# Optimization experiments

Measured on AMD Instinct MI355X. Metric: run time of the kernel, lower is better.

## Reference

```python
import jax, jax.numpy as jnp
import numpy as np

N, E, D, G, L = 50000, 400000, 64, 256, 4
VA, VB = 64, 8   # atom / bond feature vocab sizes
NUM_ATOM_FEATS, NUM_BOND_FEATS = 9, 3
MSG_EPS = 1e-7   # GENConv message epsilon
LN_EPS = 1e-5


def layernorm(x, g, b):
    mu = x.mean(-1, keepdims=True)
    var = x.var(-1, keepdims=True)
    return (x - mu) * jax.lax.rsqrt(var + LN_EPS) * g + b


def genconv(h, edge_emb, src, dst, W, b):
    # GENConv (aggr='softmax', t=1, mlp_layers=1):
    # msg = relu(x_j + e) + eps; per-dst per-feature softmax-weighted sum; mlp(x + m)
    msg = jax.nn.relu(h[src] + edge_emb) + MSG_EPS          # [E, D]
    mmax = jax.ops.segment_max(msg, dst, num_segments=N)    # [N, D]
    mmax = jnp.where(jnp.isfinite(mmax), mmax, 0.0)         # nodes with no in-edges
    ex = jnp.exp(msg - mmax[dst])
    denom = jax.ops.segment_sum(ex, dst, num_segments=N)
    alpha = ex / jnp.maximum(denom[dst], 1e-16)
    m = jax.ops.segment_sum(alpha * msg, dst, num_segments=N)  # [N, D]
    return (h + m) @ W + b


def setup_inputs():
    key = jax.random.key(0)
    ks = jax.random.split(key, 10)
    x = jax.random.randint(ks[0], (N, NUM_ATOM_FEATS), 0, VA)
    edge_index = jax.random.randint(ks[1], (2, E), 0, N)
    edge_attr = jax.random.randint(ks[2], (E, NUM_BOND_FEATS), 0, VB)
    batch = jnp.sort(jax.random.randint(ks[3], (N,), 0, G))
    s = 0.02
    w = 1.0 / np.sqrt(D).astype(np.float32)
    atom_emb = jax.random.normal(ks[4], (NUM_ATOM_FEATS, VA, D), jnp.float32) * s
    bond_emb = jax.random.normal(ks[5], (NUM_BOND_FEATS, VB, D), jnp.float32) * s
    gcn_W = jax.random.normal(ks[6], (L, D, D), jnp.float32) * w
    gcn_b = jnp.zeros((L, D), jnp.float32)
    norm_g = jnp.ones((L, D), jnp.float32)
    norm_b = jnp.zeros((L, D), jnp.float32)
    vn_emb = jnp.zeros((1, D), jnp.float32)  # constant-init virtualnode embedding
    vn_W1 = jax.random.normal(ks[7], (L - 1, D, D), jnp.float32) * w
    vn_b1 = jnp.zeros((L - 1, D), jnp.float32)
    vn_g1 = jnp.ones((L - 1, D), jnp.float32)
    vn_be1 = jnp.zeros((L - 1, D), jnp.float32)
    vn_W2 = jax.random.normal(ks[8], (L - 1, D, D), jnp.float32) * w
    vn_b2 = jnp.zeros((L - 1, D), jnp.float32)
    vn_g2 = jnp.ones((L - 1, D), jnp.float32)
    vn_be2 = jnp.zeros((L - 1, D), jnp.float32)
    return dict(x=x, edge_index=edge_index, edge_attr=edge_attr, batch=batch,
                atom_emb=atom_emb, bond_emb=bond_emb, gcn_W=gcn_W, gcn_b=gcn_b,
                norm_g=norm_g, norm_b=norm_b, vn_emb=vn_emb,
                vn_W1=vn_W1, vn_b1=vn_b1, vn_g1=vn_g1, vn_be1=vn_be1,
                vn_W2=vn_W2, vn_b2=vn_b2, vn_g2=vn_g2, vn_be2=vn_be2)


def reference(x, edge_index, edge_attr, batch, atom_emb, bond_emb, gcn_W, gcn_b,
              norm_g, norm_b, vn_emb, vn_W1, vn_b1, vn_g1, vn_be1,
              vn_W2, vn_b2, vn_g2, vn_be2):
    src, dst = edge_index[0], edge_index[1]
    # AtomEncoder / BondEncoder: sum of per-feature embedding lookups
    h = atom_emb[jnp.arange(NUM_ATOM_FEATS)[None, :], x].sum(1)          # [N, D]
    edge_emb = bond_emb[jnp.arange(NUM_BOND_FEATS)[None, :], edge_attr].sum(1)  # [E, D]
    vn = jnp.broadcast_to(vn_emb[0], (G, D))
    h = h + vn[batch]
    # block == 'res+' (eval mode: dropout is identity)
    h = genconv(h, edge_emb, src, dst, gcn_W[0], gcn_b[0])
    for l in range(1, L):
        h2 = jax.nn.relu(layernorm(h, norm_g[l - 1], norm_b[l - 1]))
        vt = jax.ops.segment_sum(h2, batch, num_segments=G) + vn         # global_add_pool
        vt = jax.nn.relu(layernorm(vt @ vn_W1[l - 1] + vn_b1[l - 1], vn_g1[l - 1], vn_be1[l - 1]))
        vn = jax.nn.relu(layernorm(vt @ vn_W2[l - 1] + vn_b2[l - 1], vn_g2[l - 1], vn_be2[l - 1]))
        h2 = h2 + vn[batch]
        h = genconv(h2, edge_emb, src, dst, gcn_W[l], gcn_b[l]) + h
    return layernorm(h, norm_g[L - 1], norm_b[L - 1])
```

## Files before the change

kernel.cpp:

```cpp
#include <hip/hip_runtime.h>
#include <hip/hip_bf16.h>

typedef __hip_bfloat16 bf16;

#define GNUM 256
#define LN_EPS 1e-5f
#define MSG_EPS 1e-7f

typedef float f4v __attribute__((ext_vector_type(4)));
typedef short s8v __attribute__((ext_vector_type(8)));
typedef __bf16 b8v __attribute__((ext_vector_type(8)));

template <typename V>
__device__ auto mfma_bf16_(V a, V b, f4v c, int)
    -> decltype(__builtin_amdgcn_mfma_f32_16x16x32_bf16(a, b, c, 0, 0, 0)) {
  return __builtin_amdgcn_mfma_f32_16x16x32_bf16(a, b, c, 0, 0, 0);
}
template <typename V>
__device__ f4v mfma_bf16_(V a, V b, f4v c, long) {
  return __builtin_amdgcn_mfma_f32_16x16x32_bf16(__builtin_bit_cast(s8v, a),
                                                 __builtin_bit_cast(s8v, b), c, 0, 0, 0);
}
__device__ __forceinline__ f4v mfma16(uint4 a, uint4 b, f4v c){
  return mfma_bf16_(__builtin_bit_cast(b8v, a), __builtin_bit_cast(b8v, b), c, 0);
}

__device__ __forceinline__ float bu2f(unsigned short u){
  unsigned v = ((unsigned)u) << 16; return __builtin_bit_cast(float, v);
}
__device__ __forceinline__ unsigned short f2bu(float f){
  unsigned u = __builtin_bit_cast(unsigned, f);
  return (unsigned short)((u + 0x7FFFu + ((u >> 16) & 1u)) >> 16);
}

__device__ __forceinline__ float wave_sum64(float v){
  #pragma unroll
  for (int off = 32; off > 0; off >>= 1) v += __shfl_xor(v, off, 64);
  return v;
}

struct Params15 {
  const void* src[15];
  int n[15];
  int off[15];
};

__global__ __launch_bounds__(256) void k_convert(Params15 P, int* __restrict__ flag,
                                                 float* __restrict__ dst,
                                                 int* __restrict__ counts, int nc){
  __shared__ int isf_sh;
  int tid = threadIdx.x;
  if (tid < 64){
    const unsigned short* u = (const unsigned short*)P.src[0];
    int bad = 0;
    for (int k = tid; k < 256; k += 64){
      unsigned short v = u[2*k];
      if (((v >> 7) & 0xFFu) >= 137u) bad = 1;
    }
    unsigned long long m = __ballot(bad);
    if (tid == 0) isf_sh = (m != 0ull) ? 1 : 0;
  }
  __syncthreads();
  bool isf = (isf_sh != 0);
  if (blockIdx.x == 0 && tid == 0) *flag = isf ? 1 : 0;
  for (int a = 0; a < 15; ++a){
    int n = P.n[a];
    float* d = dst + P.off[a];
    if (isf){
      const float* s = (const float*)P.src[a];
      for (int i = blockIdx.x*256 + tid; i < n; i += gridDim.x*256) d[i] = s[i];
    } else {
      const bf16* s = (const bf16*)P.src[a];
      for (int i = blockIdx.x*256 + tid; i < n; i += gridDim.x*256) d[i] = __bfloat162float(s[i]);
    }
  }
  for (int i = blockIdx.x*256 + tid; i < nc; i += gridDim.x*256) counts[i] = 0;
}

__global__ void k_count(const int* __restrict__ dst, int* __restrict__ counts, int E){
  int e = blockIdx.x*256 + threadIdx.x;
  if (e < E) atomicAdd(counts + dst[e], 1);
}

__global__ __launch_bounds__(256) void k_scan1(const int* __restrict__ counts,
                                               int* __restrict__ offs,
                                               int* __restrict__ btot, int n){
  __shared__ int wsum[4];
  int tid = threadIdx.x, w = tid >> 6, lane = tid & 63;
  int i = blockIdx.x*256 + tid;
  int v = (i < n) ? counts[i] : 0;
  int incl = v;
  #pragma unroll
  for (int off = 1; off < 64; off <<= 1){
    int t = __shfl_up(incl, off, 64);
    if (lane >= off) incl += t;
  }
  if (lane == 63) wsum[w] = incl;
  __syncthreads();
  int woff = 0;
  for (int k = 0; k < w; ++k) woff += wsum[k];
  int tot = incl + woff;
  if (i < n) offs[i+1] = tot;
  if (tid == 255) btot[blockIdx.x] = tot;
}

__global__ __launch_bounds__(256) void k_scan2(const int* __restrict__ btot,
                                               int* __restrict__ bexc, int nb){
  __shared__ int wsum[4];
  __shared__ int carry_sh;
  int tid = threadIdx.x, w = tid >> 6, lane = tid & 63;
  if (tid == 0) carry_sh = 0;
  __syncthreads();
  for (int base = 0; base < nb; base += 256){
    int i = base + tid;
    int v = (i < nb) ? btot[i] : 0;
    int incl = v;
    #pragma unroll
    for (int off = 1; off < 64; off <<= 1){
      int t = __shfl_up(incl, off, 64);
      if (lane >= off) incl += t;
    }
    if (lane == 63) wsum[w] = incl;
    __syncthreads();
    int carry = carry_sh;
    int woff = 0;
    for (int k = 0; k < w; ++k) woff += wsum[k];
    if (i < nb) bexc[i] = carry + woff + incl - v;
    __syncthreads();
    if (tid == 0) carry_sh = carry + wsum[0] + wsum[1] + wsum[2] + wsum[3];
    __syncthreads();
  }
}

__global__ void k_scan3(int* __restrict__ offs, int* __restrict__ cursor,
                        const int* __restrict__ bexc, int n){
  int i = blockIdx.x*256 + threadIdx.x;
  if (i == 0){ offs[0] = 0; cursor[0] = 0; }
  if (i < n){
    int v = offs[i+1] + bexc[blockIdx.x];
    offs[i+1] = v;
    if (i+1 < n) cursor[i+1] = v;
  }
}

__global__ void k_scatter(const int* __restrict__ src, const int* __restrict__ dst,
                          const int* __restrict__ ea, int* __restrict__ cursor,
                          int* __restrict__ payload, int E){
  int e = blockIdx.x*256 + threadIdx.x;
  if (e >= E) return;
  int d = dst[e];
  int pos = atomicAdd(cursor + d, 1);
  payload[pos] = (src[e] & 0xFFFF) | (ea[e*3] << 16) | (ea[e*3+1] << 19) | (ea[e*3+2] << 22);
}

__global__ void k_prep(const float* __restrict__ gw, unsigned short* __restrict__ Wf,
                       const int* __restrict__ batch, int* __restrict__ goffs,
                       const int* __restrict__ x, const float* __restrict__ atom_emb,
                       const float* __restrict__ vn_emb, unsigned short* __restrict__ b0,
                       int n){
  if (blockIdx.x < 64){
    int t = blockIdx.x*256 + threadIdx.x;
    int j = t & 7, lane = (t >> 3) & 63, nt = (t >> 9) & 3, kt = (t >> 11) & 1, l = t >> 12;
    int k = kt*32 + (lane >> 4)*8 + j;
    int c = nt*16 + (lane & 15);
    Wf[t] = f2bu(gw[l*4096 + k*64 + c]);
  } else if (blockIdx.x < 66){
    int g = (blockIdx.x - 64)*256 + threadIdx.x;
    if (g > GNUM) return;
    if (g == GNUM){ goffs[GNUM] = n; return; }
    int lo = 0, hi = n;
    while (lo < hi){ int mid = (lo+hi)>>1; if (batch[mid] < g) lo = mid+1; else hi = mid; }
    goffs[g] = lo;
  } else {
    int t = (blockIdx.x - 66) * 256 + threadIdx.x;
    int i = t >> 6, j = t & 63;
    if (i >= n) return;
    float acc = vn_emb[j];
    #pragma unroll
    for (int f = 0; f < 9; ++f){
      int idx = x[i*9 + f];
      acc += atom_emb[(f*64 + idx)*64 + j];
    }
    b0[t] = f2bu(acc);
  }
}

__global__ __launch_bounds__(256) void k_layer(
    const unsigned short* __restrict__ b0, const int* __restrict__ offs,
    const int* __restrict__ payload, const float* __restrict__ bond,
    const unsigned short* __restrict__ Wf, const float* __restrict__ bias,
    unsigned short* __restrict__ hres, unsigned short* __restrict__ h2b,
    void* __restrict__ finalout, const float* __restrict__ ng,
    const float* __restrict__ nb, const int* __restrict__ flag,
    int use_res, int mode, int n){
  __shared__ float Bs[1536];
  __shared__ __align__(16) unsigned short T[16][72];
  __shared__ float PS1[4][16], PS2[4][16];
  int tid = threadIdx.x;
  for (int idx = tid; idx < 1536; idx += 256) Bs[idx] = bond[idx];
  __syncthreads();
  int w = tid >> 6, j = tid & 63;
  int v0 = blockIdx.x * 16;
  int vb = v0 + w*4;

  int oidx = vb + (j < 5 ? j : 4);
  if (oidx > n) oidx = n;
  int o5 = offs[oidx];

  for (int r = 0; r < 4; ++r){
    int v = vb + r;
    float tv = 0.f;
    if (v < n){
      int e0 = __builtin_amdgcn_readfirstlane(__shfl(o5, r, 64));
      int e1 = __builtin_amdgcn_readfirstlane(__shfl(o5, r + 1, 64));
      float own = bu2f(b0[((unsigned)v << 6) + j]);
      tv = own;
      if (e1 > e0){
        float den = 0.f, num = 0.f;
        for (int e = e0; e < e1; e += 8){
          int rem = e1 - e;
          int pu[8]; float hv[8];
          #pragma unroll
          for (int u = 0; u < 8; ++u){
            int ei = (u < rem) ? e + u : e0;
            pu[u] = payload[ei];
          }
          #pragma unroll
          for (int u = 0; u < 8; ++u)
            hv[u] = bu2f(b0[((unsigned)(pu[u] & 0xFFFF) << 6) + j]);
          if (rem >= 8){
            #pragma unroll
            for (int u = 0; u < 8; ++u){
              int p = pu[u];
              float eev = Bs[((p >> 16) & 7)*64 + j]
                        + Bs[(8 + ((p >> 19) & 7))*64 + j]
                        + Bs[(16 + ((p >> 22) & 7))*64 + j];
              float mm = fmaxf(hv[u] + eev, 0.f) + MSG_EPS;
              float ex = __expf(mm);
              den += ex;
              num = fmaf(ex, mm, num);
            }
          } else {
            #pragma unroll
            for (int u = 0; u < 8; ++u){
              if (u < rem){
                int p = pu[u];
                float eev = Bs[((p >> 16) & 7)*64 + j]
                          + Bs[(8 + ((p >> 19) & 7))*64 + j]
                          + Bs[(16 + ((p >> 22) & 7))*64 + j];
                float mm = fmaxf(hv[u] + eev, 0.f) + MSG_EPS;
                float ex = __expf(mm);
                den += ex;
                num = fmaf(ex, mm, num);
              }
            }
          }
        }
        tv = own + num / fmaxf(den, 1e-16f);
      }
    }
    T[w*4 + r][j] = f2bu(tv);
  }
  __syncthreads();

  int ct = w;
  int quad = j >> 4, lm = j & 15;
  const uint4* Wfv = (const uint4*)Wf;
  uint4 B0 = Wfv[(size_t)(0*4 + ct)*64 + j];
  uint4 B1 = Wfv[(size_t)(1*4 + ct)*64 + j];
  uint4 A0 = *(const uint4*)&T[lm][8*quad];
  uint4 A1 = *(const uint4*)&T[lm][32 + 8*quad];
  f4v acc = (f4v){0.f,0.f,0.f,0.f};
  acc = mfma16(A0, B0, acc);
  acc = mfma16(A1, B1, acc);

  int col = ct*16 + lm;
  float bv = bias[col];
  float s1[4], s2[4];
  #pragma unroll
  for (int reg = 0; reg < 4; ++reg){
    int row = v0 + quad*4 + reg;
    float val = acc[reg] + bv;
    if (use_res && row < n) val += bu2f(hres[((unsigned)row << 6) + col]);
    acc[reg] = val;
    s1[reg] = val;
    s2[reg] = val*val;
  }
  #pragma unroll
  for (int reg = 0; reg < 4; ++reg){
    #pragma unroll
    for (int m = 1; m < 16; m <<= 1){
      s1[reg] += __shfl_xor(s1[reg], m, 64);
      s2[reg] += __shfl_xor(s2[reg], m, 64);
    }
  }
  if (lm == 0){
    #pragma unroll
    for (int reg = 0; reg < 4; ++reg){
      int rl = quad*4 + reg;
      PS1[ct][rl] = s1[reg];
      PS2[ct][rl] = s2[reg];
    }
  }
  __syncthreads();

  bool isf = (mode == 1) && (*flag != 0);
  #pragma unroll
  for (int reg = 0; reg < 4; ++reg){
    int rl = quad*4 + reg;
    int row = v0 + rl;
    if (row >= n) continue;
    float t1 = PS1[0][rl] + PS1[1][rl] + PS1[2][rl] + PS1[3][rl];
    float t2 = PS2[0][rl] + PS2[1][rl] + PS2[2][rl] + PS2[3][rl];
    float mu = t1 * (1.f/64.f);
    float var = fmaxf(t2 * (1.f/64.f) - mu*mu, 0.f);
    float rstd = rsqrtf(var + LN_EPS);
    float val = acc[reg];
    float y = (val - mu) * rstd * ng[col] + nb[col];
    size_t o = ((size_t)row << 6) + col;
    if (mode == 0){
      hres[o] = f2bu(val);
      h2b[o] = f2bu(fmaxf(y, 0.f));
    } else {
      if (isf) ((float*)finalout)[o] = y;
      else     ((bf16*)finalout)[o]  = __float2bfloat16(y);
    }
  }
}

__global__ __launch_bounds__(512) void k_vn(
    const unsigned short* __restrict__ h2b, const int* __restrict__ goffs,
    const float* __restrict__ vn_emb, float* __restrict__ vn,
    unsigned short* __restrict__ b0,
    const float* __restrict__ W1, const float* __restrict__ b1,
    const float* __restrict__ g1, const float* __restrict__ be1,
    const float* __restrict__ W2, const float* __restrict__ b2,
    const float* __restrict__ g2, const float* __restrict__ be2,
    int first){
  __shared__ float Ws[4096];
  __shared__ float part[8][64];
  __shared__ float rowbuf[64];
  __shared__ float vnew[64];
  int tid = threadIdx.x, w = tid >> 6, j = tid & 63, g = blockIdx.x;
  for (int idx = tid; idx < 4096; idx += 512) Ws[idx] = W1[idx];
  int r0 = goffs[g], r1 = goffs[g+1];
  float sum = 0.f;
  for (int i = r0 + w; i < r1; i += 8) sum += bu2f(h2b[((unsigned)i << 6) + j]);
  part[w][j] = sum;
  __syncthreads();
  float y = 0.f;
  if (tid < 64){
    float s = part[0][j] + part[1][j] + part[2][j] + part[3][j]
            + part[4][j] + part[5][j] + part[6][j] + part[7][j]
            + (first ? vn_emb[j] : vn[((unsigned)g << 6) + j]);
    rowbuf[j] = s;
  }
  __syncthreads();
  if (tid < 64){
    float acc = b1[j];
    #pragma unroll
    for (int k = 0; k < 64; ++k) acc = fmaf(rowbuf[k], Ws[k*64 + j], acc);
    float mu = wave_sum64(acc) * (1.f/64.f);
    float d = acc - mu;
    float var = wave_sum64(d*d) * (1.f/64.f);
    y = fmaxf(d * rsqrtf(var + LN_EPS) * g1[j] + be1[j], 0.f);
  }
  __syncthreads();
  for (int idx = tid; idx < 4096; idx += 512) Ws[idx] = W2[idx];
  if (tid < 64) rowbuf[j] = y;
  __syncthreads();
  if (tid < 64){
    float acc = b2[j];
    #pragma unroll
    for (int k = 0; k < 64; ++k) acc = fmaf(rowbuf[k], Ws[k*64 + j], acc);
    float mu = wave_sum64(acc) * (1.f/64.f);
    float d = acc - mu;
    float var = wave_sum64(d*d) * (1.f/64.f);
    float v2 = fmaxf(d * rsqrtf(var + LN_EPS) * g2[j] + be2[j], 0.f);
    vn[((unsigned)g << 6) + j] = v2;
    vnew[j] = v2;
  }
  __syncthreads();
  float vj = vnew[j];
  for (int i = r0 + w; i < r1; i += 8)
    b0[((unsigned)i << 6) + j] = f2bu(bu2f(h2b[((unsigned)i << 6) + j]) + vj);
}

extern "C" void kernel_launch(void* const* d_in, const int* in_sizes, int n_in,
                              void* d_out, int out_size, void* d_ws, size_t ws_size,
                              hipStream_t stream){
  const int* x          = (const int*)d_in[0];
  const int* edge_index = (const int*)d_in[1];
  const int* edge_attr  = (const int*)d_in[2];
  const int* batch      = (const int*)d_in[3];

  const int N = in_sizes[3];
  const int E = in_sizes[2] / 3;
  const int L = 4;

  const int P_ATOM = 0, P_BOND = 36864, P_GW = 38400, P_GB = 54784,
            P_NG = 55040, P_NB = 55296, P_VNE = 55552, P_W1 = 55616,
            P_B1 = 67904, P_G1 = 68096, P_BE1 = 68288, P_W2 = 68480,
            P_B2 = 80768, P_G2 = 80960, P_BE2 = 81152, P_END = 81344;

  char* ws = (char*)d_ws;
  size_t off = 0;
  auto alloc = [&](size_t bytes)->char*{
    char* p = ws + off; off += (bytes + 255) & ~(size_t)255; return p;
  };
  int*    flag   = (int*)alloc(256);
  float*  par    = (float*)alloc((size_t)P_END * 4);
  unsigned short* Wf  = (unsigned short*)alloc(16384 * 2);
  unsigned short* b0  = (unsigned short*)alloc((size_t)N*64*2);
  unsigned short* h2b = (unsigned short*)alloc((size_t)N*64*2);
  unsigned short* hres= (unsigned short*)alloc((size_t)N*64*2);
  int*    counts = (int*)alloc((size_t)N*4);
  int*    offs   = (int*)alloc((size_t)(N+1)*4);
  int*    cursor = (int*)alloc((size_t)N*4);
  int*    btot   = (int*)alloc(1024);
  int*    bexc   = (int*)alloc(1024);
  int*    payload= (int*)alloc((size_t)E*4);
  int*    goffs  = (int*)alloc((size_t)(GNUM+1)*4);
  float*  vn     = (float*)alloc((size_t)GNUM*64*4);
  (void)ws_size; (void)n_in; (void)out_size;

  Params15 P;
  const int poffs[15] = {P_ATOM,P_BOND,P_GW,P_GB,P_NG,P_NB,P_VNE,P_W1,P_B1,P_G1,P_BE1,P_W2,P_B2,P_G2,P_BE2};
  for (int a = 0; a < 15; ++a){ P.src[a] = d_in[4+a]; P.n[a] = in_sizes[4+a]; P.off[a] = poffs[a]; }

  int nodeGrid = (N*64 + 255) / 256;
  int nScanB   = (N + 255) / 256;
  int eGrid    = (E + 255) / 256;
  const int* srcp = edge_index;
  const int* dstp = edge_index + E;

  k_convert<<<128, 256, 0, stream>>>(P, flag, par, counts, N);
  k_count<<<eGrid, 256, 0, stream>>>(dstp, counts, E);
  k_scan1<<<nScanB, 256, 0, stream>>>(counts, offs, btot, N);
  k_scan2<<<1, 256, 0, stream>>>(btot, bexc, nScanB);
  k_scan3<<<nScanB, 256, 0, stream>>>(offs, cursor, bexc, N);
  k_scatter<<<eGrid, 256, 0, stream>>>(srcp, dstp, edge_attr, cursor, payload, E);
  k_prep<<<66 + nodeGrid, 256, 0, stream>>>(par + P_GW, Wf, batch, goffs,
                                            x, par + P_ATOM, par + P_VNE, b0, N);

  int layerGrid = (N + 15) / 16;
  for (int l = 0; l < L; ++l){
    if (l > 0){
      k_vn<<<GNUM, 512, 0, stream>>>(h2b, goffs, par + P_VNE, vn, b0,
                                     par + P_W1 + (l-1)*4096, par + P_B1 + (l-1)*64,
                                     par + P_G1 + (l-1)*64, par + P_BE1 + (l-1)*64,
                                     par + P_W2 + (l-1)*4096, par + P_B2 + (l-1)*64,
                                     par + P_G2 + (l-1)*64, par + P_BE2 + (l-1)*64,
                                     l == 1 ? 1 : 0);
    }
    int mode = (l == L-1) ? 1 : 0;
    k_layer<<<layerGrid, 256, 0, stream>>>(b0, offs, payload, par + P_BOND,
                                           Wf + (size_t)l*4096, par + P_GB + l*64,
                                           hres, h2b, d_out,
                                           par + P_NG + l*64, par + P_NB + l*64,
                                           flag, l > 0 ? 1 : 0, mode, N);
  }
}
```

Before: 356.6 us.

## Move layernorm+relu into vn kernel, drop h2b buffer, merge front-end kernels

The layer kernel no longer computes layernorm and writes the extra h2b tensor in non-final layers. It stores only the residual h, and the virtual-node kernel recomputes layernorm+relu per row with wave reductions in both of its passes. This removes a full N×64 bf16 write and read per layer, at the cost of doing the layernorm twice in k_vn. Separately, the convert and prep kernels are merged into one front kernel that reads raw inputs directly, which removes one launch and the dependency between them.

```diff
diff --git a/kernel.cpp b/kernel.cpp
--- a/kernel.cpp
+++ b/kernel.cpp
@@ -45,36 +45,86 @@
   int off[15];
 };
 
-__global__ __launch_bounds__(256) void k_convert(Params15 P, int* __restrict__ flag,
-                                                 float* __restrict__ dst,
-                                                 int* __restrict__ counts, int nc){
-  __shared__ int isf_sh;
-  int tid = threadIdx.x;
+__device__ __forceinline__ bool derive_isf(const void* atom_src, int tid, int* sh){
   if (tid < 64){
-    const unsigned short* u = (const unsigned short*)P.src[0];
+    const unsigned short* u = (const unsigned short*)atom_src;
     int bad = 0;
     for (int k = tid; k < 256; k += 64){
       unsigned short v = u[2*k];
       if (((v >> 7) & 0xFFu) >= 137u) bad = 1;
     }
     unsigned long long m = __ballot(bad);
-    if (tid == 0) isf_sh = (m != 0ull) ? 1 : 0;
-  }
-  __syncthreads();
-  bool isf = (isf_sh != 0);
-  if (blockIdx.x == 0 && tid == 0) *flag = isf ? 1 : 0;
-  for (int a = 0; a < 15; ++a){
-    int n = P.n[a];
-    float* d = dst + P.off[a];
+    if (tid == 0) *sh = (m != 0ull) ? 1 : 0;
+  }
+  __syncthreads();
+  return *sh != 0;
+}
+
+__global__ __launch_bounds__(256) void k_front(
+    Params15 P, int* __restrict__ flag, float* __restrict__ par,
+    int* __restrict__ counts,
+    const int* __restrict__ x, const int* __restrict__ batch,
+    unsigned short* __restrict__ Wf, int* __restrict__ goffs,
+    unsigned short* __restrict__ b0, int n){
+  __shared__ int isf_sh;
+  int tid = threadIdx.x, bid = blockIdx.x;
+  bool isf = derive_isf(P.src[0], tid, &isf_sh);
+
+  if (bid < 128){
+    if (bid == 0 && tid == 0) *flag = isf ? 1 : 0;
+    int stride = 128*256;
+    int gid = bid*256 + tid;
+    for (int a = 0; a < 15; ++a){
+      int nn = P.n[a];
+      float* d = par + P.off[a];
+      if (isf){
+        const float* s = (const float*)P.src[a];
+        for (int i = gid; i < nn; i += stride) d[i] = s[i];
+      } else {
+        const bf16* s = (const bf16*)P.src[a];
+        for (int i = gid; i < nn; i += stride) d[i] = __bfloat162float(s[i]);
+      }
+    }
+    for (int i = gid; i < n; i += stride) counts[i] = 0;
+  } else if (bid < 192){
+    int t = (bid - 128)*256 + tid;
+    int j = t & 7, lane = (t >> 3) & 63, nt = (t >> 9) & 3, kt = (t >> 11) & 1, l = t >> 12;
+    int k = kt*32 + (lane >> 4)*8 + j;
+    int c = nt*16 + (lane & 15);
+    int src = l*4096 + k*64 + c;
+    if (isf) Wf[t] = f2bu(((const float*)P.src[2])[src]);
+    else     Wf[t] = ((const unsigned short*)P.src[2])[src];
+  } else if (bid < 194){
+    int g = (bid - 192)*256 + tid;
+    if (g > GNUM) return;
+    if (g == GNUM){ goffs[GNUM] = n; return; }
+    int lo = 0, hi = n;
+    while (lo < hi){ int mid = (lo+hi)>>1; if (batch[mid] < g) lo = mid+1; else hi = mid; }
+    goffs[g] = lo;
+  } else {
+    int t = (bid - 194) * 256 + tid;
+    int i = t >> 6, j = t & 63;
+    if (i >= n) return;
+    float acc;
     if (isf){
-      const float* s = (const float*)P.src[a];
-      for (int i = blockIdx.x*256 + tid; i < n; i += gridDim.x*256) d[i] = s[i];
+      const float* ae = (const float*)P.src[0];
+      acc = ((const float*)P.src[6])[j];
+      #pragma unroll
+      for (int f = 0; f < 9; ++f){
+        int idx = x[i*9 + f];
+        acc += ae[(f*64 + idx)*64 + j];
+      }
     } else {
-      const bf16* s = (const bf16*)P.src[a];
-      for (int i = blockIdx.x*256 + tid; i < n; i += gridDim.x*256) d[i] = __bfloat162float(s[i]);
-    }
-  }
-  for (int i = blockIdx.x*256 + tid; i < nc; i += gridDim.x*256) counts[i] = 0;
+      const unsigned short* ae = (const unsigned short*)P.src[0];
+      acc = bu2f(((const unsigned short*)P.src[6])[j]);
+      #pragma unroll
+      for (int f = 0; f < 9; ++f){
+        int idx = x[i*9 + f];
+        acc += bu2f(ae[(f*64 + idx)*64 + j]);
+      }
+    }
+    b0[t] = f2bu(acc);
+  }
 }
 
 __global__ void k_count(const int* __restrict__ dst, int* __restrict__ counts, int E){
@@ -153,46 +203,13 @@
   payload[pos] = (src[e] & 0xFFFF) | (ea[e*3] << 16) | (ea[e*3+1] << 19) | (ea[e*3+2] << 22);
 }
 
-__global__ void k_prep(const float* __restrict__ gw, unsigned short* __restrict__ Wf,
-                       const int* __restrict__ batch, int* __restrict__ goffs,
-                       const int* __restrict__ x, const float* __restrict__ atom_emb,
-                       const float* __restrict__ vn_emb, unsigned short* __restrict__ b0,
-                       int n){
-  if (blockIdx.x < 64){
-    int t = blockIdx.x*256 + threadIdx.x;
-    int j = t & 7, lane = (t >> 3) & 63, nt = (t >> 9) & 3, kt = (t >> 11) & 1, l = t >> 12;
-    int k = kt*32 + (lane >> 4)*8 + j;
-    int c = nt*16 + (lane & 15);
-    Wf[t] = f2bu(gw[l*4096 + k*64 + c]);
-  } else if (blockIdx.x < 66){
-    int g = (blockIdx.x - 64)*256 + threadIdx.x;
-    if (g > GNUM) return;
-    if (g == GNUM){ goffs[GNUM] = n; return; }
-    int lo = 0, hi = n;
-    while (lo < hi){ int mid = (lo+hi)>>1; if (batch[mid] < g) lo = mid+1; else hi = mid; }
-    goffs[g] = lo;
-  } else {
-    int t = (blockIdx.x - 66) * 256 + threadIdx.x;
-    int i = t >> 6, j = t & 63;
-    if (i >= n) return;
-    float acc = vn_emb[j];
-    #pragma unroll
-    for (int f = 0; f < 9; ++f){
-      int idx = x[i*9 + f];
-      acc += atom_emb[(f*64 + idx)*64 + j];
-    }
-    b0[t] = f2bu(acc);
-  }
-}
-
 __global__ __launch_bounds__(256) void k_layer(
     const unsigned short* __restrict__ b0, const int* __restrict__ offs,
     const int* __restrict__ payload, const float* __restrict__ bond,
     const unsigned short* __restrict__ Wf, const float* __restrict__ bias,
-    unsigned short* __restrict__ hres, unsigned short* __restrict__ h2b,
-    void* __restrict__ finalout, const float* __restrict__ ng,
-    const float* __restrict__ nb, const int* __restrict__ flag,
-    int use_res, int mode, int n){
+    unsigned short* __restrict__ hres, void* __restrict__ finalout,
+    const float* __restrict__ ng, const float* __restrict__ nb,
+    const int* __restrict__ flag, int use_res, int mode, int n){
   __shared__ float Bs[1536];
   __shared__ __align__(16) unsigned short T[16][72];
   __shared__ float PS1[4][16], PS2[4][16];
@@ -276,16 +293,26 @@
 
   int col = ct*16 + lm;
   float bv = bias[col];
-  float s1[4], s2[4];
   #pragma unroll
   for (int reg = 0; reg < 4; ++reg){
     int row = v0 + quad*4 + reg;
     float val = acc[reg] + bv;
     if (use_res && row < n) val += bu2f(hres[((unsigned)row << 6) + col]);
     acc[reg] = val;
-    s1[reg] = val;
-    s2[reg] = val*val;
-  }
+  }
+
+  if (mode == 0){
+    #pragma unroll
+    for (int reg = 0; reg < 4; ++reg){
+      int row = v0 + quad*4 + reg;
+      if (row < n) hres[((size_t)row << 6) + col] = f2bu(acc[reg]);
+    }
+    return;
+  }
+
+  float s1[4], s2[4];
+  #pragma unroll
+  for (int reg = 0; reg < 4; ++reg){ s1[reg] = acc[reg]; s2[reg] = acc[reg]*acc[reg]; }
   #pragma unroll
   for (int reg = 0; reg < 4; ++reg){
     #pragma unroll
@@ -304,7 +331,7 @@
   }
   __syncthreads();
 
-  bool isf = (mode == 1) && (*flag != 0);
+  bool isf = (*flag != 0);
   #pragma unroll
   for (int reg = 0; reg < 4; ++reg){
     int rl = quad*4 + reg;
@@ -315,23 +342,18 @@
     float mu = t1 * (1.f/64.f);
     float var = fmaxf(t2 * (1.f/64.f) - mu*mu, 0.f);
     float rstd = rsqrtf(var + LN_EPS);
-    float val = acc[reg];
-    float y = (val - mu) * rstd * ng[col] + nb[col];
+    float y = (acc[reg] - mu) * rstd * ng[col] + nb[col];
     size_t o = ((size_t)row << 6) + col;
-    if (mode == 0){
-      hres[o] = f2bu(val);
-      h2b[o] = f2bu(fmaxf(y, 0.f));
-    } else {
-      if (isf) ((float*)finalout)[o] = y;
-      else     ((bf16*)finalout)[o]  = __float2bfloat16(y);
-    }
+    if (isf) ((float*)finalout)[o] = y;
+    else     ((bf16*)finalout)[o]  = __float2bfloat16(y);
   }
 }
 
 __global__ __launch_bounds__(512) void k_vn(
-    const unsigned short* __restrict__ h2b, const int* __restrict__ goffs,
+    const unsigned short* __restrict__ hres, const int* __restrict__ goffs,
     const float* __restrict__ vn_emb, float* __restrict__ vn,
     unsigned short* __restrict__ b0,
+    const float* __restrict__ ng, const float* __restrict__ nbb,
     const float* __restrict__ W1, const float* __restrict__ b1,
     const float* __restrict__ g1, const float* __restrict__ be1,
     const float* __restrict__ W2, const float* __restrict__ b2,
@@ -342,10 +364,17 @@
   __shared__ float rowbuf[64];
   __shared__ float vnew[64];
   int tid = threadIdx.x, w = tid >> 6, j = tid & 63, g = blockIdx.x;
+  float ngj = ng[j], nbj = nbb[j];
   for (int idx = tid; idx < 4096; idx += 512) Ws[idx] = W1[idx];
   int r0 = goffs[g], r1 = goffs[g+1];
   float sum = 0.f;
-  for (int i = r0 + w; i < r1; i += 8) sum += bu2f(h2b[((unsigned)i << 6) + j]);
+  for (int i = r0 + w; i < r1; i += 8){
+    float xv = bu2f(hres[((unsigned)i << 6) + j]);
+    float m1 = wave_sum64(xv) * (1.f/64.f);
+    float d = xv - m1;
+    float var = wave_sum64(d*d) * (1.f/64.f);
+    sum += fmaxf(d * rsqrtf(var + LN_EPS) * ngj + nbj, 0.f);
+  }
   part[w][j] = sum;
   __syncthreads();
   float y = 0.f;
@@ -382,8 +411,14 @@
   }
   __syncthreads();
   float vj = vnew[j];
-  for (int i = r0 + w; i < r1; i += 8)
-    b0[((unsigned)i << 6) + j] = f2bu(bu2f(h2b[((unsigned)i << 6) + j]) + vj);
+  for (int i = r0 + w; i < r1; i += 8){
+    float xv = bu2f(hres[((unsigned)i << 6) + j]);
+    float m1 = wave_sum64(xv) * (1.f/64.f);
+    float d = xv - m1;
+    float var = wave_sum64(d*d) * (1.f/64.f);
+    float h2 = fmaxf(d * rsqrtf(var + LN_EPS) * ngj + nbj, 0.f);
+    b0[((unsigned)i << 6) + j] = f2bu(h2 + vj);
+  }
 }
 
 extern "C" void kernel_launch(void* const* d_in, const int* in_sizes, int n_in,
@@ -412,7 +447,6 @@
   float*  par    = (float*)alloc((size_t)P_END * 4);
   unsigned short* Wf  = (unsigned short*)alloc(16384 * 2);
   unsigned short* b0  = (unsigned short*)alloc((size_t)N*64*2);
-  unsigned short* h2b = (unsigned short*)alloc((size_t)N*64*2);
   unsigned short* hres= (unsigned short*)alloc((size_t)N*64*2);
   int*    counts = (int*)alloc((size_t)N*4);
   int*    offs   = (int*)alloc((size_t)(N+1)*4);
@@ -434,19 +468,19 @@
   const int* srcp = edge_index;
   const int* dstp = edge_index + E;
 
-  k_convert<<<128, 256, 0, stream>>>(P, flag, par, counts, N);
+  k_front<<<194 + nodeGrid, 256, 0, stream>>>(P, flag, par, counts, x, batch,
+                                              Wf, goffs, b0, N);
   k_count<<<eGrid, 256, 0, stream>>>(dstp, counts, E);
   k_scan1<<<nScanB, 256, 0, stream>>>(counts, offs, btot, N);
   k_scan2<<<1, 256, 0, stream>>>(btot, bexc, nScanB);
   k_scan3<<<nScanB, 256, 0, stream>>>(offs, cursor, bexc, N);
   k_scatter<<<eGrid, 256, 0, stream>>>(srcp, dstp, edge_attr, cursor, payload, E);
-  k_prep<<<66 + nodeGrid, 256, 0, stream>>>(par + P_GW, Wf, batch, goffs,
-                                            x, par + P_ATOM, par + P_VNE, b0, N);
 
   int layerGrid = (N + 15) / 16;
   for (int l = 0; l < L; ++l){
     if (l > 0){
-      k_vn<<<GNUM, 512, 0, stream>>>(h2b, goffs, par + P_VNE, vn, b0,
+      k_vn<<<GNUM, 512, 0, stream>>>(hres, goffs, par + P_VNE, vn, b0,
+                                     par + P_NG + (l-1)*64, par + P_NB + (l-1)*64,
                                      par + P_W1 + (l-1)*4096, par + P_B1 + (l-1)*64,
                                      par + P_G1 + (l-1)*64, par + P_BE1 + (l-1)*64,
                                      par + P_W2 + (l-1)*4096, par + P_B2 + (l-1)*64,
@@ -456,7 +490,7 @@
     int mode = (l == L-1) ? 1 : 0;
     k_layer<<<layerGrid, 256, 0, stream>>>(b0, offs, payload, par + P_BOND,
                                            Wf + (size_t)l*4096, par + P_GB + l*64,
-                                           hres, h2b, d_out,
+                                           hres, d_out,
                                            par + P_NG + l*64, par + P_NB + l*64,
                                            flag, l > 0 ? 1 : 0, mode, N);
   }
```

After: 415.0 us. +16.4%, slower.
